# Kernel tuning notes

Hardware: AMD Instinct MI355X
Metric: run time of the kernel (lower is better)

The kernel has to match this reference:

```python
import jax, jax.numpy as jnp
import numpy as np

N_NODES = 50000
N_EDGES = 1600000
D_IN = 128
D_OUT = 128


def setup_inputs() -> dict:
    key = jax.random.key(0)
    ks = jax.random.split(key, 8)
    feat = jax.random.normal(ks[0], (N_NODES, D_IN), dtype=jnp.float32)
    src = jax.random.randint(ks[1], (N_EDGES,), 0, N_NODES, dtype=jnp.int32)
    dst = jax.random.randint(ks[2], (N_EDGES,), 0, N_NODES, dtype=jnp.int32)
    # Xavier-uniform-ish init for the two linear layers
    lim = float(np.sqrt(6.0 / (D_IN + D_OUT))) * float(np.sqrt(2.0))  # gain=relu
    W_self = jax.random.uniform(ks[3], (D_OUT, D_IN), jnp.float32, -lim, lim)
    b_self = jnp.zeros((D_OUT,), jnp.float32)
    W_neigh = jax.random.uniform(ks[4], (D_OUT, D_IN), jnp.float32, -lim, lim)
    b_neigh = jnp.zeros((D_OUT,), jnp.float32)
    return {
        "feat": feat, "src": src, "dst": dst,
        "W_self": W_self, "b_self": b_self,
        "W_neigh": W_neigh, "b_neigh": b_neigh,
    }


def reference(feat, src, dst, W_self, b_self, W_neigh, b_neigh):
    """GraphSAGE 'mean' aggregator, eval mode (feat_drop=0).

    in_feats == out_feats -> lin_before_mp is False:
      h_neigh = fc_neigh(mean_{u in N(v)} feat[u])
      rst     = fc_self(feat[v]) + h_neigh
    Zero in-degree nodes get a zero neighbor vector (DGL mean semantics).
    """
    n = feat.shape[0]
    msg = feat[src]                                            # [E, D_in] gather
    agg = jax.ops.segment_sum(msg, dst, num_segments=n)        # [N, D_in] scatter-add
    deg = jax.ops.segment_sum(jnp.ones_like(src, feat.dtype), dst, num_segments=n)
    h_neigh = agg / jnp.maximum(deg, 1.0)[:, None]             # segment mean
    h_neigh = h_neigh @ W_neigh.T + b_neigh                    # fc_neigh
    h_self = feat @ W_self.T + b_self                          # fc_self
    return h_self + h_neigh
```

## Files before the change

kernel.cpp:

```cpp
#include <hip/hip_runtime.h>
#include <hip/hip_fp16.h>

#define D 128
#define BLOCK 256
#define CAP 96
#define NPB 32
#define CBINSH 7
#define NCBINS 392
#define BCAP 6144
#define CHUNK 8192

typedef __attribute__((ext_vector_type(2))) float floatx2;
typedef __attribute__((ext_vector_type(4))) float floatx4;
typedef __attribute__((ext_vector_type(8))) _Float16 half8;

union U4H8 { uint4 u; half8 h; };

__device__ inline void addq(float* acc, unsigned int q) {
    floatx2 lo = __builtin_amdgcn_cvt_pk_f32_fp8(q, false);
    floatx2 hi = __builtin_amdgcn_cvt_pk_f32_fp8(q, true);
    acc[0] += lo[0]; acc[1] += lo[1]; acc[2] += hi[0]; acc[3] += hi[1];
}

__device__ inline void add16(float* acc, uint4 r) {
    addq(acc + 0,  r.x);
    addq(acc + 4,  r.y);
    addq(acc + 8,  r.z);
    addq(acc + 12, r.w);
}

__global__ __launch_bounds__(256) void sage_prep_bin(
    const int* __restrict__ src, const int* __restrict__ dst,
    int* __restrict__ bin_cursor, unsigned int* __restrict__ bins, int n_edges,
    int nbin_blocks,
    const float4* __restrict__ feat4, unsigned int* __restrict__ feat8, int n4,
    int ncvt_blocks,
    const float* __restrict__ W_self, const float* __restrict__ W_neigh,
    const float* __restrict__ b_self, const float* __restrict__ b_neigh,
    unsigned int* __restrict__ wcat2, float* __restrict__ biascat)
{
    __shared__ int hist[NCBINS];
    __shared__ int base[NCBINS];
    int b = blockIdx.x, t = threadIdx.x;

    if (b < nbin_blocks) {
        for (int i = t; i < NCBINS; i += 256) hist[i] = 0;
        __syncthreads();

        int e0 = b * CHUNK;
        int eend = min(e0 + CHUNK, n_edges);

        for (int i = e0 + t; i < eend; i += 256)
            atomicAdd(&hist[dst[i] >> CBINSH], 1);
        __syncthreads();

        for (int bin = t; bin < NCBINS; bin += 256) {
            int h = hist[bin];
            base[bin] = h ? atomicAdd(&bin_cursor[bin], h) : 0;
            hist[bin] = 0;
        }
        __syncthreads();

        for (int i = e0 + t; i < eend; i += 256) {
            int d = dst[i];
            int s = src[i];
            int bin = d >> CBINSH;
            int r = atomicAdd(&hist[bin], 1);
            int pos = base[bin] + r;
            if (pos < BCAP)
                bins[(size_t)bin * BCAP + pos] =
                    ((unsigned int)(d & 127) << 16) | (unsigned int)s;
        }
    } else if (b < nbin_blocks + ncvt_blocks) {
        int i = (b - nbin_blocks) * 256 + t;
        if (i < n4) {
            float4 f = feat4[i];
            unsigned int r = __builtin_amdgcn_cvt_pk_fp8_f32(f.x, f.y, 0u, false);
            r = __builtin_amdgcn_cvt_pk_fp8_f32(f.z, f.w, r, true);
            feat8[i] = r;
        }
    } else {
        int idx = (b - nbin_blocks - ncvt_blocks) * 256 + t;
        int n = idx >> 7;
        int k = (idx & 127) * 2;
        float a, bb;
        if (k < 128) { a = W_self[n * 128 + k];        bb = W_self[n * 128 + k + 1]; }
        else         { a = W_neigh[n * 128 + k - 128]; bb = W_neigh[n * 128 + k - 127]; }
        __half2 h = __floats2half2_rn(a, bb);
        wcat2[idx] = *reinterpret_cast<unsigned int*>(&h);
        if (idx < 128) biascat[idx] = b_self[idx] + b_neigh[idx];
    }
}

__global__ __launch_bounds__(BLOCK) void sage_bucket_agg(
    const float* __restrict__ feat,
    const uint4* __restrict__ feat84,
    const unsigned int* __restrict__ bins,
    const int* __restrict__ bin_cursor,
    const uint4* __restrict__ wcat4,
    const float* __restrict__ biascat,
    float* __restrict__ out, int n_nodes)
{
    __shared__ unsigned short buck[NPB * CAP];
    __shared__ int cnt[NPB];
    __shared__ _Float16 mean_lds[NPB][136];

    int b = blockIdx.x;
    int t = threadIdx.x;
    int wave = t >> 6;
    int lane = t & 63;

    if (t < NPB) cnt[t] = 0;
    __syncthreads();
    {
        int B = b >> 2;
        int lo7 = (b & 3) * 32;
        int n_items = min(bin_cursor[B], BCAP);
        const unsigned int* bp = bins + (size_t)B * BCAP;
        for (int i = t; i < n_items; i += 256) {
            unsigned int it = bp[i];
            int d7 = (int)(it >> 16);
            unsigned int rel = (unsigned int)(d7 - lo7);
            if (rel < (unsigned int)NPB) {
                int c = atomicAdd(&cnt[rel], 1);
                if (c < CAP) buck[rel * CAP + c] = (unsigned short)(it & 0xFFFFu);
            }
        }
    }
    __syncthreads();

    int v0 = b * NPB;

    {
        int g = (lane >> 4) & 3;
        int eo = (lane >> 3) & 1;
        int h = lane & 7;
        int lo = 2 * g + eo;

        for (int v = wave; v < NPB; v += 4) {
            int node = v0 + v;
            if (node >= n_nodes) break;
            int deg = cnt[v];
            int cv = min(deg, CAP);
            const unsigned short* bk = &buck[v * CAP];

            float acc[16];
            #pragma unroll
            for (int i = 0; i < 16; ++i) acc[i] = 0.0f;

            int e = 0;
            for (; e + 32 <= cv; e += 32) {
                int s0 = bk[e + lo];
                int s1 = bk[e + 8 + lo];
                int s2 = bk[e + 16 + lo];
                int s3 = bk[e + 24 + lo];
                uint4 r0 = feat84[(size_t)s0 * 8 + h];
                uint4 r1 = feat84[(size_t)s1 * 8 + h];
                uint4 r2 = feat84[(size_t)s2 * 8 + h];
                uint4 r3 = feat84[(size_t)s3 * 8 + h];
                add16(acc, r0); add16(acc, r1); add16(acc, r2); add16(acc, r3);
            }
            #pragma unroll
            for (int k = 0; k < 4; ++k) {
                int idx = e + 8 * k + lo;
                if (idx < cv) {
                    uint4 r = feat84[(size_t)bk[idx] * 8 + h];
                    add16(acc, r);
                }
            }

            #pragma unroll
            for (int i = 0; i < 16; ++i) {
                acc[i] += __shfl_xor(acc[i], 8);
                acc[i] += __shfl_xor(acc[i], 16);
                acc[i] += __shfl_xor(acc[i], 32);
            }
            if (lane < 8) {
                float inv = 1.0f / fmaxf((float)deg, 1.0f);
                unsigned int p[8];
                #pragma unroll
                for (int i = 0; i < 8; ++i) {
                    __half2 hh = __floats2half2_rn(acc[2 * i] * inv, acc[2 * i + 1] * inv);
                    p[i] = *reinterpret_cast<unsigned int*>(&hh);
                }
                uint4 lo4 = { p[0], p[1], p[2], p[3] };
                uint4 hi4 = { p[4], p[5], p[6], p[7] };
                uint4* xp = (uint4*)&mean_lds[v][h * 16];
                xp[0] = lo4;
                xp[1] = hi4;
            }
        }
    }
    __syncthreads();

    {
        int rg = wave >> 1;
        int ch = wave & 1;
        int m16 = lane & 15;
        int kq = lane >> 4;
        int m = v0 + rg * 16 + m16;
        int msafe = (m < n_nodes) ? m : 0;

        half8 a[8];
        const float4* fp = (const float4*)(feat + (size_t)msafe * D);
        #pragma unroll
        for (int kt = 0; kt < 4; ++kt) {
            float4 f0 = fp[kt * 8 + kq * 2];
            float4 f1 = fp[kt * 8 + kq * 2 + 1];
            half8 hh;
            hh[0] = (_Float16)f0.x; hh[1] = (_Float16)f0.y;
            hh[2] = (_Float16)f0.z; hh[3] = (_Float16)f0.w;
            hh[4] = (_Float16)f1.x; hh[5] = (_Float16)f1.y;
            hh[6] = (_Float16)f1.z; hh[7] = (_Float16)f1.w;
            a[kt] = hh;
        }
        const uint4* mrow = (const uint4*)&mean_lds[rg * 16 + m16][0];
        #pragma unroll
        for (int kt = 0; kt < 4; ++kt) {
            U4H8 u; u.u = mrow[kt * 4 + kq];
            a[4 + kt] = u.h;
        }

        #pragma unroll
        for (int cc = 0; cc < 4; ++cc) {
            int ct = ch * 4 + cc;
            floatx4 acc = { 0.f, 0.f, 0.f, 0.f };
            #pragma unroll
            for (int kt = 0; kt < 8; ++kt) {
                U4H8 w; w.u = wcat4[(size_t)(ct * 16 + m16) * 32 + kt * 4 + kq];
                acc = __builtin_amdgcn_mfma_f32_16x16x32_f16(a[kt], w.h, acc, 0, 0, 0);
            }
            float bias = biascat[ct * 16 + m16];
            #pragma unroll
            for (int i = 0; i < 4; ++i) {
                int r = v0 + rg * 16 + kq * 4 + i;
                if (r < n_nodes)
                    out[(size_t)r * D + ct * 16 + m16] = acc[i] + bias;
            }
        }
    }
}

extern "C" void kernel_launch(void* const* d_in, const int* in_sizes, int n_in,
                              void* d_out, int out_size, void* d_ws, size_t ws_size,
                              hipStream_t stream)
{
    const float* feat    = (const float*)d_in[0];
    const int*   src     = (const int*)d_in[1];
    const int*   dst     = (const int*)d_in[2];
    const float* W_self  = (const float*)d_in[3];
    const float* b_self  = (const float*)d_in[4];
    const float* W_neigh = (const float*)d_in[5];
    const float* b_neigh = (const float*)d_in[6];
    float* out = (float*)d_out;

    int n_nodes = in_sizes[0] / D;
    int n_edges = in_sizes[1];

    unsigned int* bins = (unsigned int*)d_ws;
    unsigned int* feat8 = bins + (size_t)NCBINS * BCAP;
    unsigned int* wcat = feat8 + (size_t)n_nodes * (D / 4);
    float* biascat = (float*)(wcat + 128 * 128);
    int* bin_cursor = (int*)(biascat + 128);

    int n4 = n_nodes * (D / 4);
    int ncvt = (n4 + 255) / 256;
    int nbinblk = (n_edges + CHUNK - 1) / CHUNK;
    int naggblk = (n_nodes + NPB - 1) / NPB;

    hipMemsetAsync(bin_cursor, 0, NCBINS * sizeof(int), stream);
    sage_prep_bin<<<nbinblk + ncvt + 64, 256, 0, stream>>>(
        src, dst, bin_cursor, bins, n_edges, nbinblk,
        (const float4*)feat, feat8, n4, ncvt,
        W_self, W_neigh, b_self, b_neigh, wcat, biascat);
    sage_bucket_agg<<<naggblk, BLOCK, 0, stream>>>(
        feat, (const uint4*)feat8, bins, bin_cursor,
        (const uint4*)wcat, biascat, out, n_nodes);
}
```

Before: 200.4 us.

## Replace global coarse binning with per-chunk counting sort and offset table

Each prep block now counting-sorts its 8192-edge chunk in shared memory by 32-node group, using an LDS prefix scan. It writes the sorted chunk and a per-chunk offset table, which removes the global bin cursors, their memset and the global atomics. Each aggregation block then reads only its own group's slice from every chunk, instead of scanning a 128-node bin and throwing away three quarters of the items. The cost is a heavier prep kernel with 1024-thread blocks, a multi-step scan with many barriers and a 1.6MB offset table. The aggregation gather also becomes a short serial loop per chunk, with scattered, non-coalesced reads.

After: 179.0 us. 1.12x faster.

```diff
diff --git a/kernel.cpp b/kernel.cpp
--- a/kernel.cpp
+++ b/kernel.cpp
@@ -3,11 +3,11 @@
 
 #define D 128
 #define BLOCK 256
+#define BLOCK1 1024
 #define CAP 96
 #define NPB 32
-#define CBINSH 7
-#define NCBINS 392
-#define BCAP 6144
+#define NPBSH 5
+#define NFBW 2048
 #define CHUNK 8192
 
 typedef __attribute__((ext_vector_type(2))) float floatx2;
@@ -29,9 +29,9 @@
     addq(acc + 12, r.w);
 }
 
-__global__ __launch_bounds__(256) void sage_prep_bin(
+__global__ __launch_bounds__(BLOCK1) void sage_prep_binsort(
     const int* __restrict__ src, const int* __restrict__ dst,
-    int* __restrict__ bin_cursor, unsigned int* __restrict__ bins, int n_edges,
+    unsigned int* __restrict__ bins2, int* __restrict__ offtab, int n_edges,
     int nbin_blocks,
     const float4* __restrict__ feat4, unsigned int* __restrict__ feat8, int n4,
     int ncvt_blocks,
@@ -39,40 +39,55 @@
     const float* __restrict__ b_self, const float* __restrict__ b_neigh,
     unsigned int* __restrict__ wcat2, float* __restrict__ biascat)
 {
-    __shared__ int hist[NCBINS];
-    __shared__ int base[NCBINS];
+    __shared__ unsigned int items[CHUNK];
+    __shared__ int hist[NFBW];
+    __shared__ int aux[BLOCK1];
     int b = blockIdx.x, t = threadIdx.x;
 
     if (b < nbin_blocks) {
-        for (int i = t; i < NCBINS; i += 256) hist[i] = 0;
+        hist[t] = 0; hist[t + 1024] = 0;
         __syncthreads();
 
         int e0 = b * CHUNK;
         int eend = min(e0 + CHUNK, n_edges);
 
-        for (int i = e0 + t; i < eend; i += 256)
-            atomicAdd(&hist[dst[i] >> CBINSH], 1);
-        __syncthreads();
-
-        for (int bin = t; bin < NCBINS; bin += 256) {
-            int h = hist[bin];
-            base[bin] = h ? atomicAdd(&bin_cursor[bin], h) : 0;
-            hist[bin] = 0;
-        }
-        __syncthreads();
-
-        for (int i = e0 + t; i < eend; i += 256) {
+        for (int i = e0 + t; i < eend; i += BLOCK1)
+            atomicAdd(&hist[dst[i] >> NPBSH], 1);
+        __syncthreads();
+
+        int s0 = hist[2 * t], s1 = hist[2 * t + 1];
+        int local = s0 + s1;
+        aux[t] = local;
+        __syncthreads();
+        for (int dd = 1; dd < BLOCK1; dd <<= 1) {
+            int v = (t >= dd) ? aux[t - dd] : 0;
+            __syncthreads();
+            aux[t] += v;
+            __syncthreads();
+        }
+        int excl = aux[t] - local;
+        hist[2 * t] = excl;
+        hist[2 * t + 1] = excl + s0;
+        __syncthreads();
+
+        offtab[(size_t)b * NFBW + t]        = hist[t];
+        offtab[(size_t)b * NFBW + 1024 + t] = hist[1024 + t];
+        __syncthreads();
+
+        for (int i = e0 + t; i < eend; i += BLOCK1) {
             int d = dst[i];
             int s = src[i];
-            int bin = d >> CBINSH;
-            int r = atomicAdd(&hist[bin], 1);
-            int pos = base[bin] + r;
-            if (pos < BCAP)
-                bins[(size_t)bin * BCAP + pos] =
-                    ((unsigned int)(d & 127) << 16) | (unsigned int)s;
-        }
+            int pos = atomicAdd(&hist[d >> NPBSH], 1);
+            items[pos] = ((unsigned int)(d & (NPB - 1)) << 16) | (unsigned int)s;
+        }
+        __syncthreads();
+
+        uint4* gb = (uint4*)(bins2 + (size_t)b * CHUNK);
+        const uint4* lb = (const uint4*)items;
+        gb[t] = lb[t];
+        gb[1024 + t] = lb[1024 + t];
     } else if (b < nbin_blocks + ncvt_blocks) {
-        int i = (b - nbin_blocks) * 256 + t;
+        int i = (b - nbin_blocks) * BLOCK1 + t;
         if (i < n4) {
             float4 f = feat4[i];
             unsigned int r = __builtin_amdgcn_cvt_pk_fp8_f32(f.x, f.y, 0u, false);
@@ -80,26 +95,28 @@
             feat8[i] = r;
         }
     } else {
-        int idx = (b - nbin_blocks - ncvt_blocks) * 256 + t;
-        int n = idx >> 7;
-        int k = (idx & 127) * 2;
-        float a, bb;
-        if (k < 128) { a = W_self[n * 128 + k];        bb = W_self[n * 128 + k + 1]; }
-        else         { a = W_neigh[n * 128 + k - 128]; bb = W_neigh[n * 128 + k - 127]; }
-        __half2 h = __floats2half2_rn(a, bb);
-        wcat2[idx] = *reinterpret_cast<unsigned int*>(&h);
-        if (idx < 128) biascat[idx] = b_self[idx] + b_neigh[idx];
+        int idx = (b - nbin_blocks - ncvt_blocks) * BLOCK1 + t;
+        if (idx < 16384) {
+            int n = idx >> 7;
+            int k = (idx & 127) * 2;
+            float a, bb;
+            if (k < 128) { a = W_self[n * 128 + k];        bb = W_self[n * 128 + k + 1]; }
+            else         { a = W_neigh[n * 128 + k - 128]; bb = W_neigh[n * 128 + k - 127]; }
+            __half2 h = __floats2half2_rn(a, bb);
+            wcat2[idx] = *reinterpret_cast<unsigned int*>(&h);
+            if (idx < 128) biascat[idx] = b_self[idx] + b_neigh[idx];
+        }
     }
 }
 
 __global__ __launch_bounds__(BLOCK) void sage_bucket_agg(
     const float* __restrict__ feat,
     const uint4* __restrict__ feat84,
-    const unsigned int* __restrict__ bins,
-    const int* __restrict__ bin_cursor,
+    const unsigned int* __restrict__ bins2,
+    const int* __restrict__ offtab,
     const uint4* __restrict__ wcat4,
     const float* __restrict__ biascat,
-    float* __restrict__ out, int n_nodes)
+    float* __restrict__ out, int n_nodes, int nbin_blocks)
 {
     __shared__ unsigned short buck[NPB * CAP];
     __shared__ int cnt[NPB];
@@ -112,19 +129,15 @@
 
     if (t < NPB) cnt[t] = 0;
     __syncthreads();
-    {
-        int B = b >> 2;
-        int lo7 = (b & 3) * 32;
-        int n_items = min(bin_cursor[B], BCAP);
-        const unsigned int* bp = bins + (size_t)B * BCAP;
-        for (int i = t; i < n_items; i += 256) {
+    for (int s = t; s < nbin_blocks; s += BLOCK) {
+        int o0 = offtab[(size_t)s * NFBW + b];
+        int o1 = offtab[(size_t)s * NFBW + b + 1];
+        const unsigned int* bp = bins2 + (size_t)s * CHUNK;
+        for (int i = o0; i < o1; ++i) {
             unsigned int it = bp[i];
-            int d7 = (int)(it >> 16);
-            unsigned int rel = (unsigned int)(d7 - lo7);
-            if (rel < (unsigned int)NPB) {
-                int c = atomicAdd(&cnt[rel], 1);
-                if (c < CAP) buck[rel * CAP + c] = (unsigned short)(it & 0xFFFFu);
-            }
+            int rel = (int)(it >> 16);
+            int c = atomicAdd(&cnt[rel], 1);
+            if (c < CAP) buck[rel * CAP + c] = (unsigned short)(it & 0xFFFFu);
         }
     }
     __syncthreads();
@@ -257,23 +270,24 @@
     int n_nodes = in_sizes[0] / D;
     int n_edges = in_sizes[1];
 
-    unsigned int* bins = (unsigned int*)d_ws;
-    unsigned int* feat8 = bins + (size_t)NCBINS * BCAP;
+    int nbinblk = (n_edges + CHUNK - 1) / CHUNK;
+
+    unsigned int* bins2 = (unsigned int*)d_ws;
+    int* offtab = (int*)(bins2 + (size_t)nbinblk * CHUNK);
+    unsigned int* feat8 = (unsigned int*)(offtab + (size_t)nbinblk * NFBW);
     unsigned int* wcat = feat8 + (size_t)n_nodes * (D / 4);
     float* biascat = (float*)(wcat + 128 * 128);
-    int* bin_cursor = (int*)(biascat + 128);
 
     int n4 = n_nodes * (D / 4);
-    int ncvt = (n4 + 255) / 256;
-    int nbinblk = (n_edges + CHUNK - 1) / CHUNK;
+    int ncvt = (n4 + BLOCK1 - 1) / BLOCK1;
+    int nwcat = 16;
     int naggblk = (n_nodes + NPB - 1) / NPB;
 
-    hipMemsetAsync(bin_cursor, 0, NCBINS * sizeof(int), stream);
-    sage_prep_bin<<<nbinblk + ncvt + 64, 256, 0, stream>>>(
-        src, dst, bin_cursor, bins, n_edges, nbinblk,
+    sage_prep_binsort<<<nbinblk + ncvt + nwcat, BLOCK1, 0, stream>>>(
+        src, dst, bins2, offtab, n_edges, nbinblk,
         (const float4*)feat, feat8, n4, ncvt,
         W_self, W_neigh, b_self, b_neigh, wcat, biascat);
     sage_bucket_agg<<<naggblk, BLOCK, 0, stream>>>(
-        feat, (const uint4*)feat8, bins, bin_cursor,
-        (const uint4*)wcat, biascat, out, n_nodes);
-}
+        feat, (const uint4*)feat8, bins2, offtab,
+        (const uint4*)wcat, biascat, out, n_nodes, nbinblk);
+}
```
